# Performance work log

Hardware: AMD Instinct MI355X
Metric: run time of the kernel (lower is better)

Reference implementation:

```python
import jax, jax.numpy as jnp
import numpy as np

B, D, A, R = 256, 1024, 1024, 8  # batch, feat_dim, ada_dim, rank
I = A  # inter_dim defaults to ada_dim
LN_EPS = 1e-5


def setup_inputs() -> dict:
    key = jax.random.key(0)
    ks = jax.random.split(key, 5)
    return {
        "x": jax.random.normal(ks[0], (B, D), jnp.float32),
        "ada_emb": jax.random.normal(ks[1], (B, A), jnp.float32),
        "base_layer": jax.random.normal(ks[2], (D, D), jnp.float32) * 0.02,
        "ln_gamma": jnp.ones((A,), jnp.float32),
        "ln_beta": jnp.zeros((A,), jnp.float32),
        "W1": jax.random.normal(ks[3], (A, I), jnp.float32) * 0.02,
        "b1": jnp.zeros((I,), jnp.float32),
        "W2": jax.random.normal(ks[4], (I, D * R * 2), jnp.float32) * 0.02,
        "b2": jnp.zeros((D * R * 2,), jnp.float32),
    }


def reference(x, ada_emb, base_layer, ln_gamma, ln_beta, W1, b1, W2, b2):
    Bc, Dc = x.shape
    # norm_cond: LayerNorm over ada_dim
    mu = jnp.mean(ada_emb, axis=-1, keepdims=True)
    var = jnp.var(ada_emb, axis=-1, keepdims=True)
    cond = (ada_emb - mu) * jax.lax.rsqrt(var + LN_EPS) * ln_gamma + ln_beta
    # gen_weight: Linear -> GELU (exact, erf) -> Linear
    h = jax.nn.gelu(cond @ W1 + b1, approximate=False)
    w = h @ W2 + b2                      # [B, 2*D*R]
    x_a, x_b = jnp.split(w, 2, axis=-1)
    x_a = x_a.reshape(Bc, Dc, R)         # [B, D, R]
    x_b = x_b.reshape(Bc, Dc, R)         # [B, D, R]
    # per-sample low-rank weight added to the shared base layer
    layer = base_layer[None, :, :] + jnp.einsum('bdr,bkr->bdk', x_a, x_b)  # [B, D, D]
    out = jnp.einsum('bc,bco->bo', x, layer)
    return x + out  # residual=True
```

## Files before the change

kernel.cpp:

```cpp
#include <hip/hip_runtime.h>
#include <math.h>

#define BB 256
#define DD 1024
#define AA 1024
#define RR 8
#define II 1024
#define NOUT (2*DD*RR)
#define LN_EPS 1e-5f

typedef __attribute__((ext_vector_type(8))) short bf16x8;
typedef __attribute__((ext_vector_type(8))) unsigned short ushort8;
typedef __attribute__((ext_vector_type(4))) float f32x4;

typedef const __attribute__((address_space(1))) unsigned int gu32_t;
typedef __attribute__((address_space(3))) unsigned int lu32_t;

__device__ __forceinline__ void glds16(void* lds, const void* g) {
    __builtin_amdgcn_global_load_lds((gu32_t*)g, (lu32_t*)lds, 16, 0, 0);
}

__device__ __forceinline__ f32x4 mfma16(bf16x8 a, bf16x8 b, f32x4 c) {
    return __builtin_amdgcn_mfma_f32_16x16x32_bf16(a, b, c, 0, 0, 0);
}

__device__ __forceinline__ unsigned short f2bf(float x) {
    unsigned int u = __float_as_uint(x);
    unsigned int r = (u + 0x7fffu + ((u >> 16) & 1u)) >> 16;
    return (unsigned short)r;
}
__device__ __forceinline__ float bf2f(unsigned short b) {
    return __uint_as_float(((unsigned int)b) << 16);
}
__device__ __forceinline__ void split2(float x, unsigned short& hi, unsigned short& lo) {
    hi = f2bf(x);
    lo = f2bf(x - bf2f(hi));
}

__device__ __forceinline__ float gelu_exact(float v) {
    return 0.5f * v * (1.0f + erff(v * 0.70710678118654752f));
}

__device__ __forceinline__ void bar() {
    __builtin_amdgcn_sched_barrier(0);
    __builtin_amdgcn_s_barrier();
    __builtin_amdgcn_sched_barrier(0);
}

__global__ __launch_bounds__(256) void ln_split_kernel(const float* __restrict__ ada,
                                                       const float* __restrict__ xp,
                                                       const float* __restrict__ gamma,
                                                       const float* __restrict__ beta,
                                                       char* __restrict__ c_t,
                                                       char* __restrict__ x_t) {
    const int b = blockIdx.x;
    const int tid = threadIdx.x;
    const float4 v = ((const float4*)(ada + (size_t)b * AA))[tid];

    float s  = v.x + v.y + v.z + v.w;
    float ss = v.x * v.x + v.y * v.y + v.z * v.z + v.w * v.w;
    #pragma unroll
    for (int off = 32; off; off >>= 1) {
        s  += __shfl_down(s, off);
        ss += __shfl_down(ss, off);
    }
    __shared__ float red[2][4];
    const int wid = tid >> 6, lane = tid & 63;
    if (lane == 0) { red[0][wid] = s; red[1][wid] = ss; }
    __syncthreads();
    __shared__ float stats[2];
    if (tid == 0) {
        float S  = red[0][0] + red[0][1] + red[0][2] + red[0][3];
        float SS = red[1][0] + red[1][1] + red[1][2] + red[1][3];
        float mu  = S * (1.0f / AA);
        float var = SS * (1.0f / AA) - mu * mu;
        stats[0] = mu;
        stats[1] = rsqrtf(var + LN_EPS);
    }
    __syncthreads();
    const float mu = stats[0], inv = stats[1];
    const float4 g  = ((const float4*)gamma)[tid];
    const float4 be = ((const float4*)beta)[tid];

    const int k0 = tid * 4;
    const int mbh = (b >> 4) & 1;
    const size_t img = ((size_t)(b >> 5) * 16 + (k0 >> 6)) * 8192;
    const int inoff = ((k0 >> 3) & 7) * 256 + (b & 15) * 16 + (k0 & 7) * 2;

    float o[4];
    o[0] = (v.x - mu) * inv * g.x + be.x;
    o[1] = (v.y - mu) * inv * g.y + be.y;
    o[2] = (v.z - mu) * inv * g.z + be.z;
    o[3] = (v.w - mu) * inv * g.w + be.w;
    ushort4 H, L;
    split2(o[0], H.x, L.x); split2(o[1], H.y, L.y);
    split2(o[2], H.z, L.z); split2(o[3], H.w, L.w);
    *(ushort4*)(c_t + img + (0 * 2 + mbh) * 2048 + inoff) = H;
    *(ushort4*)(c_t + img + (1 * 2 + mbh) * 2048 + inoff) = L;

    const float4 xv = ((const float4*)(xp + (size_t)b * DD))[tid];
    split2(xv.x, H.x, L.x); split2(xv.y, H.y, L.y);
    split2(xv.z, H.z, L.z); split2(xv.w, H.w, L.w);
    *(ushort4*)(x_t + img + (0 * 2 + mbh) * 2048 + inoff) = H;
    *(ushort4*)(x_t + img + (1 * 2 + mbh) * 2048 + inoff) = L;
}

__global__ __launch_bounds__(256) void gemm_small(const char* __restrict__ x_t,
                                                  const char* __restrict__ c_t,
                                                  const float* __restrict__ base,
                                                  const float* __restrict__ W1,
                                                  const float* __restrict__ b1,
                                                  float* __restrict__ outy,
                                                  char* __restrict__ h_t) {
    __shared__ __align__(16) char As[2][8192];
    __shared__ __align__(16) char Bs[2][16384];

    const int z = blockIdx.z;
    const char* __restrict__ At = z ? c_t : x_t;
    const float* __restrict__ Bsrc = z ? W1 : base;

    const int tid = threadIdx.x;
    const int bn = blockIdx.x * 64;
    const int bm = blockIdx.y * 32;
    const int wid = tid >> 6, l = tid & 63;
    const int kg = l >> 4, lr16 = (l & 15) * 16;

    f32x4 acc[2];
    acc[0] = (f32x4)0.0f; acc[1] = (f32x4)0.0f;

    const int sn = tid & 63;
    const int sk0 = (tid >> 6) * 16;
    const int s_nb = sn >> 4, s_l16 = (sn & 15) * 16;

    float v[16];

    #define SB_LOAD(KT)                                                          \
        _Pragma("unroll")                                                        \
        for (int j = 0; j < 16; j++)                                             \
            v[j] = Bsrc[(size_t)((KT) * 64 + sk0 + j) * 1024 + bn + sn];

    #define SB_WRITE(BUF)                                                        \
        _Pragma("unroll")                                                        \
        for (int h2 = 0; h2 < 2; h2++) {                                         \
            const int kidx = (sk0 >> 3) + h2;                                    \
            ushort8 H, L;                                                        \
            _Pragma("unroll")                                                    \
            for (int j = 0; j < 8; j++) { unsigned short hh, ll;                 \
                split2(v[h2 * 8 + j], hh, ll); H[j] = hh; L[j] = ll; }           \
            *(ushort8*)(Bs[BUF] + ((0*4 + s_nb)*8 + kidx)*256 + s_l16) = H;      \
            *(ushort8*)(Bs[BUF] + ((1*4 + s_nb)*8 + kidx)*256 + s_l16) = L;      \
        }

    #define SA_GLDS(BUF, KT)                                                     \
        {                                                                        \
            const char* ib = At + ((size_t)(bm >> 5) * 16 + (KT)) * 8192;        \
            _Pragma("unroll")                                                    \
            for (int c = 0; c < 2; c++) {                                        \
                const int ch = wid * 2 + c;                                      \
                glds16(As[BUF] + ch * 1024, ib + ch * 1024 + l * 16);            \
            }                                                                    \
        }

    #define S_COMPUTE(BUF)                                                       \
        _Pragma("unroll")                                                        \
        for (int s2 = 0; s2 < 2; s2++) {                                         \
            bf16x8 a[2][2], bbf[2];                                              \
            _Pragma("unroll")                                                    \
            for (int pl = 0; pl < 2; pl++) {                                     \
                _Pragma("unroll")                                                \
                for (int mi = 0; mi < 2; mi++)                                   \
                    a[pl][mi] = *(const bf16x8*)(As[BUF] +                       \
                        ((pl*2 + mi)*8 + s2*4 + kg)*256 + lr16);                 \
                bbf[pl] = *(const bf16x8*)(Bs[BUF] +                             \
                        ((pl*4 + wid)*8 + s2*4 + kg)*256 + lr16);                \
            }                                                                    \
            __builtin_amdgcn_s_setprio(1);                                       \
            _Pragma("unroll")                                                    \
            for (int mi = 0; mi < 2; mi++) {                                     \
                acc[mi] = mfma16(a[0][mi], bbf[0], acc[mi]);                     \
                acc[mi] = mfma16(a[0][mi], bbf[1], acc[mi]);                     \
                acc[mi] = mfma16(a[1][mi], bbf[0], acc[mi]);                     \
            }                                                                    \
            __builtin_amdgcn_s_setprio(0);                                       \
        }

    SB_LOAD(0);
    SA_GLDS(0, 0);
    SB_WRITE(0);
    asm volatile("s_waitcnt lgkmcnt(0)" ::: "memory");
    bar();

    for (int t = 0; t < 16; ++t) {
        const int cur = t & 1;
        if (t < 15) {
            SB_LOAD(t + 1);
            SA_GLDS(cur ^ 1, t + 1);
            asm volatile("s_waitcnt vmcnt(18)" ::: "memory");
        } else {
            asm volatile("s_waitcnt vmcnt(0)" ::: "memory");
        }
        bar();
        S_COMPUTE(cur);
        if (t < 15) {
            SB_WRITE(cur ^ 1);
        }
        asm volatile("s_waitcnt lgkmcnt(0)" ::: "memory");
        bar();
    }

    #pragma unroll
    for (int mi = 0; mi < 2; mi++) {
        const int row0 = bm + mi * 16 + kg * 4;
        const int col  = bn + wid * 16 + (l & 15);
        #pragma unroll
        for (int j = 0; j < 4; j++) {
            float val = acc[mi][j];
            const int row = row0 + j;
            if (z == 0) {
                outy[(size_t)row * 1024 + col] = val;
            } else {
                float g = gelu_exact(val + b1[col]);
                unsigned short hi, lo;
                split2(g, hi, lo);
                char* ib = h_t + ((size_t)(row >> 7) * 32 + (col >> 5)) * 16384;
                const int inoff = (((row >> 4) & 7) * 4 + ((col >> 3) & 3)) * 256
                                + (row & 15) * 16 + (col & 7) * 2;
                *(unsigned short*)(ib + 0 * 8192 + inoff) = hi;
                *(unsigned short*)(ib + 1 * 8192 + inoff) = lo;
            }
        }
    }
    #undef SB_LOAD
    #undef SB_WRITE
    #undef SA_GLDS
    #undef S_COMPUTE
}

__global__ __launch_bounds__(256) void gemm_big(const char* __restrict__ h_t,
                                                const float* __restrict__ Bm,
                                                const float* __restrict__ bias,
                                                float* __restrict__ Cm) {
    __shared__ __align__(16) char As[2][16384];
    __shared__ __align__(16) char Bs[2][8192];

    const int hw = blockIdx.x;
    const int swz = ((hw & 7) << 6) + (hw >> 3);
    const int bn = (swz >> 1) * 64;
    const int bm = (swz & 1) * 128;

    const int tid = threadIdx.x;
    const int wid = tid >> 6, l = tid & 63;
    const int wm = wid >> 1, wn = wid & 1;
    const int kg = l >> 4, lr16 = (l & 15) * 16;

    f32x4 acc[4][2];
    #pragma unroll
    for (int i = 0; i < 4; i++) { acc[i][0] = (f32x4)0.0f; acc[i][1] = (f32x4)0.0f; }

    const int sn = tid & 63;
    const int skc = tid >> 6;
    const int s_nb = sn >> 4, s_l16 = (sn & 15) * 16;

    float v[8];

    #define GB_LOAD(KT)                                                          \
        _Pragma("unroll")                                                        \
        for (int j = 0; j < 8; j++)                                              \
            v[j] = Bm[(size_t)((KT) * 32 + skc * 8 + j) * NOUT + bn + sn];

    #define GB_WRITE(BUF)                                                        \
        {                                                                        \
            ushort8 H, L;                                                        \
            _Pragma("unroll")                                                    \
            for (int j = 0; j < 8; j++) { unsigned short hh, ll;                 \
                split2(v[j], hh, ll); H[j] = hh; L[j] = ll; }                    \
            *(ushort8*)(Bs[BUF] + ((0*4 + s_nb)*4 + skc)*256 + s_l16) = H;       \
            *(ushort8*)(Bs[BUF] + ((1*4 + s_nb)*4 + skc)*256 + s_l16) = L;       \
        }

    #define GA_GLDS(BUF, KT)                                                     \
        {                                                                        \
            const char* ib = h_t + ((size_t)(bm >> 7) * 32 + (KT)) * 16384;      \
            _Pragma("unroll")                                                    \
            for (int c = 0; c < 4; c++) {                                        \
                const int ch = wid * 4 + c;                                      \
                glds16(As[BUF] + ch * 1024, ib + ch * 1024 + l * 16);            \
            }                                                                    \
        }

    #define G_COMPUTE(BUF)                                                       \
        {                                                                        \
            bf16x8 a[2][4], bbf[2][2];                                           \
            _Pragma("unroll")                                                    \
            for (int pl = 0; pl < 2; pl++) {                                     \
                _Pragma("unroll")                                                \
                for (int mi = 0; mi < 4; mi++)                                   \
                    a[pl][mi] = *(const bf16x8*)(As[BUF] +                       \
                        ((pl*8 + wm*4 + mi)*4 + kg)*256 + lr16);                 \
                _Pragma("unroll")                                                \
                for (int ni = 0; ni < 2; ni++)                                   \
                    bbf[pl][ni] = *(const bf16x8*)(Bs[BUF] +                     \
                        ((pl*4 + wn*2 + ni)*4 + kg)*256 + lr16);                 \
            }                                                                    \
            __builtin_amdgcn_s_setprio(1);                                       \
            _Pragma("unroll")                                                    \
            for (int mi = 0; mi < 4; mi++) {                                     \
                _Pragma("unroll")                                                \
                for (int ni = 0; ni < 2; ni++) {                                 \
                    acc[mi][ni] = mfma16(a[0][mi], bbf[0][ni], acc[mi][ni]);     \
                    acc[mi][ni] = mfma16(a[0][mi], bbf[1][ni], acc[mi][ni]);     \
                    acc[mi][ni] = mfma16(a[1][mi], bbf[0][ni], acc[mi][ni]);     \
                }                                                                \
            }                                                                    \
            __builtin_amdgcn_s_setprio(0);                                       \
        }

    GB_LOAD(0);
    GA_GLDS(0, 0);
    GB_WRITE(0);
    asm volatile("s_waitcnt lgkmcnt(0)" ::: "memory");
    bar();

    for (int t = 0; t < 32; ++t) {
        const int cur = t & 1;
        if (t < 31) {
            GB_LOAD(t + 1);
            GA_GLDS(cur ^ 1, t + 1);
            asm volatile("s_waitcnt vmcnt(12)" ::: "memory");
        } else {
            asm volatile("s_waitcnt vmcnt(0)" ::: "memory");
        }
        bar();
        G_COMPUTE(cur);
        if (t < 31) {
            GB_WRITE(cur ^ 1);
        }
        asm volatile("s_waitcnt lgkmcnt(0)" ::: "memory");
        bar();
    }

    #pragma unroll
    for (int mi = 0; mi < 4; mi++) {
        #pragma unroll
        for (int ni = 0; ni < 2; ni++) {
            const int row0 = bm + wm * 64 + mi * 16 + kg * 4;
            const int col  = bn + wn * 32 + ni * 16 + (l & 15);
            const float bv = bias[col];
            #pragma unroll
            for (int j = 0; j < 4; j++)
                Cm[(size_t)(row0 + j) * NOUT + col] = acc[mi][ni][j] + bv;
        }
    }
    #undef GB_LOAD
    #undef GB_WRITE
    #undef GA_GLDS
    #undef G_COMPUTE
}

__global__ __launch_bounds__(256) void tail_kernel(const float* __restrict__ x,
                                                   const float* __restrict__ w,
                                                   float* __restrict__ out) {
    const int b = blockIdx.x;
    const int tid = threadIdx.x;
    const float* wa = w + (size_t)b * NOUT;
    const float4 xv = ((const float4*)(x + (size_t)b * DD))[tid];
    const float xs[4] = {xv.x, xv.y, xv.z, xv.w};

    float acc[RR] = {};
    #pragma unroll
    for (int i = 0; i < 4; i++) {
        const int c = tid * 4 + i;
        const float4 w0 = *(const float4*)&wa[c * RR];
        const float4 w1 = *(const float4*)&wa[c * RR + 4];
        acc[0] = fmaf(xs[i], w0.x, acc[0]);
        acc[1] = fmaf(xs[i], w0.y, acc[1]);
        acc[2] = fmaf(xs[i], w0.z, acc[2]);
        acc[3] = fmaf(xs[i], w0.w, acc[3]);
        acc[4] = fmaf(xs[i], w1.x, acc[4]);
        acc[5] = fmaf(xs[i], w1.y, acc[5]);
        acc[6] = fmaf(xs[i], w1.z, acc[6]);
        acc[7] = fmaf(xs[i], w1.w, acc[7]);
    }
    __shared__ float red[4][RR];
    __shared__ float trs[RR];
    const int wid = tid >> 6, lane = tid & 63;
    #pragma unroll
    for (int r = 0; r < RR; r++) {
        float vv = acc[r];
        #pragma unroll
        for (int off = 32; off; off >>= 1) vv += __shfl_down(vv, off);
        if (lane == 0) red[wid][r] = vv;
    }
    __syncthreads();
    if (tid < RR) trs[tid] = red[0][tid] + red[1][tid] + red[2][tid] + red[3][tid];
    __syncthreads();

    float tr[RR];
    #pragma unroll
    for (int r = 0; r < RR; r++) tr[r] = trs[r];

    const float* wb = wa + DD * RR;
    const int o0 = tid * 4;
    const float4 yv = *(const float4*)&out[(size_t)b * DD + o0];

    float vals[4];
    #pragma unroll
    for (int i = 0; i < 4; i++) {
        const float4 w0 = *(const float4*)&wb[(o0 + i) * RR];
        const float4 w1 = *(const float4*)&wb[(o0 + i) * RR + 4];
        vals[i] = tr[0] * w0.x + tr[1] * w0.y + tr[2] * w0.z + tr[3] * w0.w
                + tr[4] * w1.x + tr[5] * w1.y + tr[6] * w1.z + tr[7] * w1.w;
    }
    float4 o;
    o.x = xv.x + yv.x + vals[0];
    o.y = xv.y + yv.y + vals[1];
    o.z = xv.z + yv.z + vals[2];
    o.w = xv.w + yv.w + vals[3];
    *(float4*)&out[(size_t)b * DD + o0] = o;
}

extern "C" void kernel_launch(void* const* d_in, const int* in_sizes, int n_in,
                              void* d_out, int out_size, void* d_ws, size_t ws_size,
                              hipStream_t stream) {
    const float* x     = (const float*)d_in[0];
    const float* ada   = (const float*)d_in[1];
    const float* base  = (const float*)d_in[2];
    const float* gamma = (const float*)d_in[3];
    const float* beta  = (const float*)d_in[4];
    const float* W1    = (const float*)d_in[5];
    const float* b1    = (const float*)d_in[6];
    const float* W2    = (const float*)d_in[7];
    const float* b2    = (const float*)d_in[8];
    float* out = (float*)d_out;

    char* wsb = (char*)d_ws;
    float* w  = (float*)(wsb);
    char* h_t = wsb + 16777216;
    char* x_t = wsb + 17825792;
    char* c_t = wsb + 18874368;

    ln_split_kernel<<<BB, 256, 0, stream>>>(ada, x, gamma, beta, c_t, x_t);

    gemm_small<<<dim3(1024 / 64, BB / 32, 2), 256, 0, stream>>>(
        x_t, c_t, base, W1, b1, out, h_t);

    gemm_big<<<512, 256, 0, stream>>>(h_t, W2, b2, w);

    tail_kernel<<<BB, 256, 0, stream>>>(x, w, out);
}
```

Measured before the change: 178.6 us.

## Fuse four kernels into one cooperative persistent kernel with grid syncs

Replaces the four separate launches (layernorm/split, small GEMMs, big GEMM, tail) with a single cooperative kernel of 512 blocks that runs each stage in turn, separated by grid-wide syncs. Shared memory is unioned into one 48KB buffer, and launch bounds ask for 2 blocks per CU. The aim is to remove per-launch overhead and inter-kernel gaps. In exchange it adds grid barrier cost and idles half the blocks in the stages that use only 256, and occupancy limits could lower GEMM throughput.

```diff
diff --git a/kernel.cpp b/kernel.cpp
--- a/kernel.cpp
+++ b/kernel.cpp
@@ -1,5 +1,8 @@
 #include <hip/hip_runtime.h>
+#include <hip/hip_cooperative_groups.h>
 #include <math.h>
+
+namespace cg = cooperative_groups;
 
 #define BB 256
 #define DD 1024
@@ -16,8 +19,8 @@
 typedef const __attribute__((address_space(1))) unsigned int gu32_t;
 typedef __attribute__((address_space(3))) unsigned int lu32_t;
 
-__device__ __forceinline__ void glds16(void* lds, const void* g) {
-    __builtin_amdgcn_global_load_lds((gu32_t*)g, (lu32_t*)lds, 16, 0, 0);
+__device__ __forceinline__ void glds16(void* ldsp, const void* g) {
+    __builtin_amdgcn_global_load_lds((gu32_t*)g, (lu32_t*)ldsp, 16, 0, 0);
 }
 
 __device__ __forceinline__ f32x4 mfma16(bf16x8 a, bf16x8 b, f32x4 c) {
@@ -47,376 +50,366 @@
     __builtin_amdgcn_sched_barrier(0);
 }
 
-__global__ __launch_bounds__(256) void ln_split_kernel(const float* __restrict__ ada,
-                                                       const float* __restrict__ xp,
-                                                       const float* __restrict__ gamma,
-                                                       const float* __restrict__ beta,
-                                                       char* __restrict__ c_t,
-                                                       char* __restrict__ x_t) {
-    const int b = blockIdx.x;
+__global__ __launch_bounds__(256, 2) void fused_all(
+    const float* __restrict__ xp, const float* __restrict__ ada,
+    const float* __restrict__ base, const float* __restrict__ gamma,
+    const float* __restrict__ beta, const float* __restrict__ W1,
+    const float* __restrict__ b1, const float* __restrict__ W2,
+    const float* __restrict__ b2, float* __restrict__ out,
+    float* __restrict__ w, char* __restrict__ h_t,
+    char* __restrict__ x_t, char* __restrict__ c_t)
+{
+    __shared__ __align__(16) char lds[49152];
+    cg::grid_group grid = cg::this_grid();
+    const int bid = blockIdx.x;
     const int tid = threadIdx.x;
-    const float4 v = ((const float4*)(ada + (size_t)b * AA))[tid];
-
-    float s  = v.x + v.y + v.z + v.w;
-    float ss = v.x * v.x + v.y * v.y + v.z * v.z + v.w * v.w;
-    #pragma unroll
-    for (int off = 32; off; off >>= 1) {
-        s  += __shfl_down(s, off);
-        ss += __shfl_down(ss, off);
+
+    if (bid < 256) {
+        const int b = bid;
+        float* red   = (float*)lds;
+        float* stats = (float*)lds + 8;
+        const float4 v = ((const float4*)(ada + (size_t)b * AA))[tid];
+
+        float s  = v.x + v.y + v.z + v.w;
+        float ss = v.x * v.x + v.y * v.y + v.z * v.z + v.w * v.w;
+        #pragma unroll
+        for (int off = 32; off; off >>= 1) {
+            s  += __shfl_down(s, off);
+            ss += __shfl_down(ss, off);
+        }
+        const int wd = tid >> 6, lane = tid & 63;
+        if (lane == 0) { red[wd] = s; red[4 + wd] = ss; }
+        __syncthreads();
+        if (tid == 0) {
+            float S  = red[0] + red[1] + red[2] + red[3];
+            float SS = red[4] + red[5] + red[6] + red[7];
+            float mu  = S * (1.0f / AA);
+            float var = SS * (1.0f / AA) - mu * mu;
+            stats[0] = mu;
+            stats[1] = rsqrtf(var + LN_EPS);
+        }
+        __syncthreads();
+        const float mu = stats[0], inv = stats[1];
+        const float4 g  = ((const float4*)gamma)[tid];
+        const float4 be = ((const float4*)beta)[tid];
+
+        const int k0 = tid * 4;
+        const int mbh = (b >> 4) & 1;
+        const size_t img = ((size_t)(b >> 5) * 16 + (k0 >> 6)) * 8192;
+        const int inoff = ((k0 >> 3) & 7) * 256 + (b & 15) * 16 + (k0 & 7) * 2;
+
+        float o[4];
+        o[0] = (v.x - mu) * inv * g.x + be.x;
+        o[1] = (v.y - mu) * inv * g.y + be.y;
+        o[2] = (v.z - mu) * inv * g.z + be.z;
+        o[3] = (v.w - mu) * inv * g.w + be.w;
+        ushort4 H, L;
+        split2(o[0], H.x, L.x); split2(o[1], H.y, L.y);
+        split2(o[2], H.z, L.z); split2(o[3], H.w, L.w);
+        *(ushort4*)(c_t + img + (0 * 2 + mbh) * 2048 + inoff) = H;
+        *(ushort4*)(c_t + img + (1 * 2 + mbh) * 2048 + inoff) = L;
+
+        const float4 xv = ((const float4*)(xp + (size_t)b * DD))[tid];
+        split2(xv.x, H.x, L.x); split2(xv.y, H.y, L.y);
+        split2(xv.z, H.z, L.z); split2(xv.w, H.w, L.w);
+        *(ushort4*)(x_t + img + (0 * 2 + mbh) * 2048 + inoff) = H;
+        *(ushort4*)(x_t + img + (1 * 2 + mbh) * 2048 + inoff) = L;
     }
-    __shared__ float red[2][4];
-    const int wid = tid >> 6, lane = tid & 63;
-    if (lane == 0) { red[0][wid] = s; red[1][wid] = ss; }
-    __syncthreads();
-    __shared__ float stats[2];
-    if (tid == 0) {
-        float S  = red[0][0] + red[0][1] + red[0][2] + red[0][3];
-        float SS = red[1][0] + red[1][1] + red[1][2] + red[1][3];
-        float mu  = S * (1.0f / AA);
-        float var = SS * (1.0f / AA) - mu * mu;
-        stats[0] = mu;
-        stats[1] = rsqrtf(var + LN_EPS);
-    }
-    __syncthreads();
-    const float mu = stats[0], inv = stats[1];
-    const float4 g  = ((const float4*)gamma)[tid];
-    const float4 be = ((const float4*)beta)[tid];
-
-    const int k0 = tid * 4;
-    const int mbh = (b >> 4) & 1;
-    const size_t img = ((size_t)(b >> 5) * 16 + (k0 >> 6)) * 8192;
-    const int inoff = ((k0 >> 3) & 7) * 256 + (b & 15) * 16 + (k0 & 7) * 2;
-
-    float o[4];
-    o[0] = (v.x - mu) * inv * g.x + be.x;
-    o[1] = (v.y - mu) * inv * g.y + be.y;
-    o[2] = (v.z - mu) * inv * g.z + be.z;
-    o[3] = (v.w - mu) * inv * g.w + be.w;
-    ushort4 H, L;
-    split2(o[0], H.x, L.x); split2(o[1], H.y, L.y);
-    split2(o[2], H.z, L.z); split2(o[3], H.w, L.w);
-    *(ushort4*)(c_t + img + (0 * 2 + mbh) * 2048 + inoff) = H;
-    *(ushort4*)(c_t + img + (1 * 2 + mbh) * 2048 + inoff) = L;
-
-    const float4 xv = ((const float4*)(xp + (size_t)b * DD))[tid];
-    split2(xv.x, H.x, L.x); split2(xv.y, H.y, L.y);
-    split2(xv.z, H.z, L.z); split2(xv.w, H.w, L.w);
-    *(ushort4*)(x_t + img + (0 * 2 + mbh) * 2048 + inoff) = H;
-    *(ushort4*)(x_t + img + (1 * 2 + mbh) * 2048 + inoff) = L;
-}
-
-__global__ __launch_bounds__(256) void gemm_small(const char* __restrict__ x_t,
-                                                  const char* __restrict__ c_t,
-                                                  const float* __restrict__ base,
-                                                  const float* __restrict__ W1,
-                                                  const float* __restrict__ b1,
-                                                  float* __restrict__ outy,
-                                                  char* __restrict__ h_t) {
-    __shared__ __align__(16) char As[2][8192];
-    __shared__ __align__(16) char Bs[2][16384];
-
-    const int z = blockIdx.z;
-    const char* __restrict__ At = z ? c_t : x_t;
-    const float* __restrict__ Bsrc = z ? W1 : base;
-
-    const int tid = threadIdx.x;
-    const int bn = blockIdx.x * 64;
-    const int bm = blockIdx.y * 32;
-    const int wid = tid >> 6, l = tid & 63;
-    const int kg = l >> 4, lr16 = (l & 15) * 16;
-
-    f32x4 acc[2];
-    acc[0] = (f32x4)0.0f; acc[1] = (f32x4)0.0f;
-
-    const int sn = tid & 63;
-    const int sk0 = (tid >> 6) * 16;
-    const int s_nb = sn >> 4, s_l16 = (sn & 15) * 16;
-
-    float v[16];
-
-    #define SB_LOAD(KT)                                                          \
-        _Pragma("unroll")                                                        \
-        for (int j = 0; j < 16; j++)                                             \
-            v[j] = Bsrc[(size_t)((KT) * 64 + sk0 + j) * 1024 + bn + sn];
-
-    #define SB_WRITE(BUF)                                                        \
-        _Pragma("unroll")                                                        \
-        for (int h2 = 0; h2 < 2; h2++) {                                         \
-            const int kidx = (sk0 >> 3) + h2;                                    \
-            ushort8 H, L;                                                        \
-            _Pragma("unroll")                                                    \
-            for (int j = 0; j < 8; j++) { unsigned short hh, ll;                 \
-                split2(v[h2 * 8 + j], hh, ll); H[j] = hh; L[j] = ll; }           \
-            *(ushort8*)(Bs[BUF] + ((0*4 + s_nb)*8 + kidx)*256 + s_l16) = H;      \
-            *(ushort8*)(Bs[BUF] + ((1*4 + s_nb)*8 + kidx)*256 + s_l16) = L;      \
-        }
-
-    #define SA_GLDS(BUF, KT)                                                     \
-        {                                                                        \
-            const char* ib = At + ((size_t)(bm >> 5) * 16 + (KT)) * 8192;        \
-            _Pragma("unroll")                                                    \
-            for (int c = 0; c < 2; c++) {                                        \
-                const int ch = wid * 2 + c;                                      \
-                glds16(As[BUF] + ch * 1024, ib + ch * 1024 + l * 16);            \
-            }                                                                    \
-        }
-
-    #define S_COMPUTE(BUF)                                                       \
-        _Pragma("unroll")                                                        \
-        for (int s2 = 0; s2 < 2; s2++) {                                         \
-            bf16x8 a[2][2], bbf[2];                                              \
-            _Pragma("unroll")                                                    \
-            for (int pl = 0; pl < 2; pl++) {                                     \
-                _Pragma("unroll")                                                \
-                for (int mi = 0; mi < 2; mi++)                                   \
-                    a[pl][mi] = *(const bf16x8*)(As[BUF] +                       \
-                        ((pl*2 + mi)*8 + s2*4 + kg)*256 + lr16);                 \
-                bbf[pl] = *(const bf16x8*)(Bs[BUF] +                             \
-                        ((pl*4 + wid)*8 + s2*4 + kg)*256 + lr16);                \
-            }                                                                    \
-            __builtin_amdgcn_s_setprio(1);                                       \
-            _Pragma("unroll")                                                    \
-            for (int mi = 0; mi < 2; mi++) {                                     \
-                acc[mi] = mfma16(a[0][mi], bbf[0], acc[mi]);                     \
-                acc[mi] = mfma16(a[0][mi], bbf[1], acc[mi]);                     \
-                acc[mi] = mfma16(a[1][mi], bbf[0], acc[mi]);                     \
-            }                                                                    \
-            __builtin_amdgcn_s_setprio(0);                                       \
-        }
-
-    SB_LOAD(0);
-    SA_GLDS(0, 0);
-    SB_WRITE(0);
-    asm volatile("s_waitcnt lgkmcnt(0)" ::: "memory");
-    bar();
-
-    for (int t = 0; t < 16; ++t) {
-        const int cur = t & 1;
-        if (t < 15) {
-            SB_LOAD(t + 1);
-            SA_GLDS(cur ^ 1, t + 1);
-            asm volatile("s_waitcnt vmcnt(18)" ::: "memory");
-        } else {
-            asm volatile("s_waitcnt vmcnt(0)" ::: "memory");
-        }
-        bar();
-        S_COMPUTE(cur);
-        if (t < 15) {
-            SB_WRITE(cur ^ 1);
-        }
+    grid.sync();
+
+    if (bid < 256) {
+        const int z = bid >> 7;
+        const char* __restrict__ At = z ? c_t : x_t;
+        const float* __restrict__ Bsrc = z ? W1 : base;
+        const int bn = (bid & 15) * 64;
+        const int bm = ((bid >> 4) & 7) * 32;
+        const int wd = tid >> 6, l = tid & 63;
+        const int kg = l >> 4, lr16 = (l & 15) * 16;
+
+        f32x4 acc[2];
+        acc[0] = (f32x4)0.0f; acc[1] = (f32x4)0.0f;
+
+        const int sn = tid & 63;
+        const int sk0 = (tid >> 6) * 16;
+        const int s_nb = sn >> 4, s_l16 = (sn & 15) * 16;
+        float v[16];
+
+        #define SB_LOAD(KT)                                                          \
+            _Pragma("unroll")                                                        \
+            for (int j = 0; j < 16; j++)                                             \
+                v[j] = Bsrc[(size_t)((KT) * 64 + sk0 + j) * 1024 + bn + sn];
+
+        #define SB_WRITE(BUF)                                                        \
+            _Pragma("unroll")                                                        \
+            for (int h2 = 0; h2 < 2; h2++) {                                         \
+                const int kidx = (sk0 >> 3) + h2;                                    \
+                ushort8 H, L;                                                        \
+                _Pragma("unroll")                                                    \
+                for (int j = 0; j < 8; j++) { unsigned short hh, ll;                 \
+                    split2(v[h2 * 8 + j], hh, ll); H[j] = hh; L[j] = ll; }           \
+                *(ushort8*)(lds + 16384 + (BUF)*16384 + ((0*4 + s_nb)*8 + kidx)*256 + s_l16) = H; \
+                *(ushort8*)(lds + 16384 + (BUF)*16384 + ((1*4 + s_nb)*8 + kidx)*256 + s_l16) = L; \
+            }
+
+        #define SA_GLDS(BUF, KT)                                                     \
+            {                                                                        \
+                const char* ib = At + ((size_t)(bm >> 5) * 16 + (KT)) * 8192;        \
+                _Pragma("unroll")                                                    \
+                for (int c = 0; c < 2; c++) {                                        \
+                    const int ch = wd * 2 + c;                                       \
+                    glds16(lds + (BUF)*8192 + ch * 1024, ib + ch * 1024 + l * 16);   \
+                }                                                                    \
+            }
+
+        #define S_COMPUTE(BUF)                                                       \
+            _Pragma("unroll")                                                        \
+            for (int s2 = 0; s2 < 2; s2++) {                                         \
+                bf16x8 a[2][2], bbf[2];                                              \
+                _Pragma("unroll")                                                    \
+                for (int pl = 0; pl < 2; pl++) {                                     \
+                    _Pragma("unroll")                                                \
+                    for (int mi = 0; mi < 2; mi++)                                   \
+                        a[pl][mi] = *(const bf16x8*)(lds + (BUF)*8192 +              \
+                            ((pl*2 + mi)*8 + s2*4 + kg)*256 + lr16);                 \
+                    bbf[pl] = *(const bf16x8*)(lds + 16384 + (BUF)*16384 +           \
+                            ((pl*4 + wd)*8 + s2*4 + kg)*256 + lr16);                 \
+                }                                                                    \
+                __builtin_amdgcn_s_setprio(1);                                       \
+                _Pragma("unroll")                                                    \
+                for (int mi = 0; mi < 2; mi++) {                                     \
+                    acc[mi] = mfma16(a[0][mi], bbf[0], acc[mi]);                     \
+                    acc[mi] = mfma16(a[0][mi], bbf[1], acc[mi]);                     \
+                    acc[mi] = mfma16(a[1][mi], bbf[0], acc[mi]);                     \
+                }                                                                    \
+                __builtin_amdgcn_s_setprio(0);                                       \
+            }
+
+        SB_LOAD(0);
+        SA_GLDS(0, 0);
+        SB_WRITE(0);
         asm volatile("s_waitcnt lgkmcnt(0)" ::: "memory");
         bar();
+
+        for (int t = 0; t < 16; ++t) {
+            const int cur = t & 1;
+            if (t < 15) {
+                SB_LOAD(t + 1);
+                SA_GLDS(cur ^ 1, t + 1);
+                asm volatile("s_waitcnt vmcnt(18)" ::: "memory");
+            } else {
+                asm volatile("s_waitcnt vmcnt(0)" ::: "memory");
+            }
+            bar();
+            S_COMPUTE(cur);
+            if (t < 15) {
+                SB_WRITE(cur ^ 1);
+            }
+            asm volatile("s_waitcnt lgkmcnt(0)" ::: "memory");
+            bar();
+        }
+
+        #pragma unroll
+        for (int mi = 0; mi < 2; mi++) {
+            const int row0 = bm + mi * 16 + kg * 4;
+            const int col  = bn + wd * 16 + (l & 15);
+            #pragma unroll
+            for (int j = 0; j < 4; j++) {
+                float val = acc[mi][j];
+                const int row = row0 + j;
+                if (z == 0) {
+                    out[(size_t)row * 1024 + col] = val;
+                } else {
+                    float gv = gelu_exact(val + b1[col]);
+                    unsigned short hi, lo;
+                    split2(gv, hi, lo);
+                    char* ib = h_t + ((size_t)(row >> 7) * 32 + (col >> 5)) * 16384;
+                    const int inoff = (((row >> 4) & 7) * 4 + ((col >> 3) & 3)) * 256
+                                    + (row & 15) * 16 + (col & 7) * 2;
+                    *(unsigned short*)(ib + 0 * 8192 + inoff) = hi;
+                    *(unsigned short*)(ib + 1 * 8192 + inoff) = lo;
+                }
+            }
+        }
+        #undef SB_LOAD
+        #undef SB_WRITE
+        #undef SA_GLDS
+        #undef S_COMPUTE
     }
-
-    #pragma unroll
-    for (int mi = 0; mi < 2; mi++) {
-        const int row0 = bm + mi * 16 + kg * 4;
-        const int col  = bn + wid * 16 + (l & 15);
-        #pragma unroll
-        for (int j = 0; j < 4; j++) {
-            float val = acc[mi][j];
-            const int row = row0 + j;
-            if (z == 0) {
-                outy[(size_t)row * 1024 + col] = val;
-            } else {
-                float g = gelu_exact(val + b1[col]);
-                unsigned short hi, lo;
-                split2(g, hi, lo);
-                char* ib = h_t + ((size_t)(row >> 7) * 32 + (col >> 5)) * 16384;
-                const int inoff = (((row >> 4) & 7) * 4 + ((col >> 3) & 3)) * 256
-                                + (row & 15) * 16 + (col & 7) * 2;
-                *(unsigned short*)(ib + 0 * 8192 + inoff) = hi;
-                *(unsigned short*)(ib + 1 * 8192 + inoff) = lo;
-            }
-        }
-    }
-    #undef SB_LOAD
-    #undef SB_WRITE
-    #undef SA_GLDS
-    #undef S_COMPUTE
-}
-
-__global__ __launch_bounds__(256) void gemm_big(const char* __restrict__ h_t,
-                                                const float* __restrict__ Bm,
-                                                const float* __restrict__ bias,
-                                                float* __restrict__ Cm) {
-    __shared__ __align__(16) char As[2][16384];
-    __shared__ __align__(16) char Bs[2][8192];
-
-    const int hw = blockIdx.x;
-    const int swz = ((hw & 7) << 6) + (hw >> 3);
-    const int bn = (swz >> 1) * 64;
-    const int bm = (swz & 1) * 128;
-
-    const int tid = threadIdx.x;
-    const int wid = tid >> 6, l = tid & 63;
-    const int wm = wid >> 1, wn = wid & 1;
-    const int kg = l >> 4, lr16 = (l & 15) * 16;
-
-    f32x4 acc[4][2];
-    #pragma unroll
-    for (int i = 0; i < 4; i++) { acc[i][0] = (f32x4)0.0f; acc[i][1] = (f32x4)0.0f; }
-
-    const int sn = tid & 63;
-    const int skc = tid >> 6;
-    const int s_nb = sn >> 4, s_l16 = (sn & 15) * 16;
-
-    float v[8];
-
-    #define GB_LOAD(KT)                                                          \
-        _Pragma("unroll")                                                        \
-        for (int j = 0; j < 8; j++)                                              \
-            v[j] = Bm[(size_t)((KT) * 32 + skc * 8 + j) * NOUT + bn + sn];
-
-    #define GB_WRITE(BUF)                                                        \
-        {                                                                        \
-            ushort8 H, L;                                                        \
-            _Pragma("unroll")                                                    \
-            for (int j = 0; j < 8; j++) { unsigned short hh, ll;                 \
-                split2(v[j], hh, ll); H[j] = hh; L[j] = ll; }                    \
-            *(ushort8*)(Bs[BUF] + ((0*4 + s_nb)*4 + skc)*256 + s_l16) = H;       \
-            *(ushort8*)(Bs[BUF] + ((1*4 + s_nb)*4 + skc)*256 + s_l16) = L;       \
-        }
-
-    #define GA_GLDS(BUF, KT)                                                     \
-        {                                                                        \
-            const char* ib = h_t + ((size_t)(bm >> 7) * 32 + (KT)) * 16384;      \
-            _Pragma("unroll")                                                    \
-            for (int c = 0; c < 4; c++) {                                        \
-                const int ch = wid * 4 + c;                                      \
-                glds16(As[BUF] + ch * 1024, ib + ch * 1024 + l * 16);            \
-            }                                                                    \
-        }
-
-    #define G_COMPUTE(BUF)                                                       \
-        {                                                                        \
-            bf16x8 a[2][4], bbf[2][2];                                           \
-            _Pragma("unroll")                                                    \
-            for (int pl = 0; pl < 2; pl++) {                                     \
-                _Pragma("unroll")                                                \
-                for (int mi = 0; mi < 4; mi++)                                   \
-                    a[pl][mi] = *(const bf16x8*)(As[BUF] +                       \
-                        ((pl*8 + wm*4 + mi)*4 + kg)*256 + lr16);                 \
-                _Pragma("unroll")                                                \
-                for (int ni = 0; ni < 2; ni++)                                   \
-                    bbf[pl][ni] = *(const bf16x8*)(Bs[BUF] +                     \
-                        ((pl*4 + wn*2 + ni)*4 + kg)*256 + lr16);                 \
-            }                                                                    \
-            __builtin_amdgcn_s_setprio(1);                                       \
-            _Pragma("unroll")                                                    \
-            for (int mi = 0; mi < 4; mi++) {                                     \
-                _Pragma("unroll")                                                \
-                for (int ni = 0; ni < 2; ni++) {                                 \
-                    acc[mi][ni] = mfma16(a[0][mi], bbf[0][ni], acc[mi][ni]);     \
-                    acc[mi][ni] = mfma16(a[0][mi], bbf[1][ni], acc[mi][ni]);     \
-                    acc[mi][ni] = mfma16(a[1][mi], bbf[0][ni], acc[mi][ni]);     \
-                }                                                                \
-            }                                                                    \
-            __builtin_amdgcn_s_setprio(0);                                       \
-        }
-
-    GB_LOAD(0);
-    GA_GLDS(0, 0);
-    GB_WRITE(0);
-    asm volatile("s_waitcnt lgkmcnt(0)" ::: "memory");
-    bar();
-
-    for (int t = 0; t < 32; ++t) {
-        const int cur = t & 1;
-        if (t < 31) {
-            GB_LOAD(t + 1);
-            GA_GLDS(cur ^ 1, t + 1);
-            asm volatile("s_waitcnt vmcnt(12)" ::: "memory");
-        } else {
-            asm volatile("s_waitcnt vmcnt(0)" ::: "memory");
-        }
-        bar();
-        G_COMPUTE(cur);
-        if (t < 31) {
-            GB_WRITE(cur ^ 1);
-        }
+    grid.sync();
+
+    {
+        const int hw = bid;
+        const int swz = ((hw & 7) << 6) + (hw >> 3);
+        const int bn = (swz >> 1) * 64;
+        const int bm = (swz & 1) * 128;
+
+        const int wd = tid >> 6, l = tid & 63;
+        const int wm = wd >> 1, wn = wd & 1;
+        const int kg = l >> 4, lr16 = (l & 15) * 16;
+
+        f32x4 acc[4][2];
+        #pragma unroll
+        for (int i = 0; i < 4; i++) { acc[i][0] = (f32x4)0.0f; acc[i][1] = (f32x4)0.0f; }
+
+        const int sn = tid & 63;
+        const int skc = tid >> 6;
+        const int s_nb = sn >> 4, s_l16 = (sn & 15) * 16;
+        float v[8];
+
+        #define GB_LOAD(KT)                                                          \
+            _Pragma("unroll")                                                        \
+            for (int j = 0; j < 8; j++)                                              \
+                v[j] = W2[(size_t)((KT) * 32 + skc * 8 + j) * NOUT + bn + sn];
+
+        #define GB_WRITE(BUF)                                                        \
+            {                                                                        \
+                ushort8 H, L;                                                        \
+                _Pragma("unroll")                                                    \
+                for (int j = 0; j < 8; j++) { unsigned short hh, ll;                 \
+                    split2(v[j], hh, ll); H[j] = hh; L[j] = ll; }                    \
+                *(ushort8*)(lds + 32768 + (BUF)*8192 + ((0*4 + s_nb)*4 + skc)*256 + s_l16) = H; \
+                *(ushort8*)(lds + 32768 + (BUF)*8192 + ((1*4 + s_nb)*4 + skc)*256 + s_l16) = L; \
+            }
+
+        #define GA_GLDS(BUF, KT)                                                     \
+            {                                                                        \
+                const char* ib = h_t + ((size_t)(bm >> 7) * 32 + (KT)) * 16384;      \
+                _Pragma("unroll")                                                    \
+                for (int c = 0; c < 4; c++) {                                        \
+                    const int ch = wd * 4 + c;                                       \
+                    glds16(lds + (BUF)*16384 + ch * 1024, ib + ch * 1024 + l * 16);  \
+                }                                                                    \
+            }
+
+        #define G_COMPUTE(BUF)                                                       \
+            {                                                                        \
+                bf16x8 a[2][4], bbf[2][2];                                           \
+                _Pragma("unroll")                                                    \
+                for (int pl = 0; pl < 2; pl++) {                                     \
+                    _Pragma("unroll")                                                \
+                    for (int mi = 0; mi < 4; mi++)                                   \
+                        a[pl][mi] = *(const bf16x8*)(lds + (BUF)*16384 +             \
+                            ((pl*8 + wm*4 + mi)*4 + kg)*256 + lr16);                 \
+                    _Pragma("unroll")                                                \
+                    for (int ni = 0; ni < 2; ni++)                                   \
+                        bbf[pl][ni] = *(const bf16x8*)(lds + 32768 + (BUF)*8192 +    \
+                            ((pl*4 + wn*2 + ni)*4 + kg)*256 + lr16);                 \
+                }                                                                    \
+                __builtin_amdgcn_s_setprio(1);                                       \
+                _Pragma("unroll")                                                    \
+                for (int mi = 0; mi < 4; mi++) {                                     \
+                    _Pragma("unroll")                                                \
+                    for (int ni = 0; ni < 2; ni++) {                                 \
+                        acc[mi][ni] = mfma16(a[0][mi], bbf[0][ni], acc[mi][ni]);     \
+                        acc[mi][ni] = mfma16(a[0][mi], bbf[1][ni], acc[mi][ni]);     \
+                        acc[mi][ni] = mfma16(a[1][mi], bbf[0][ni], acc[mi][ni]);     \
+                    }                                                                \
+                }                                                                    \
+                __builtin_amdgcn_s_setprio(0);                                       \
+            }
+
+        GB_LOAD(0);
+        GA_GLDS(0, 0);
+        GB_WRITE(0);
         asm volatile("s_waitcnt lgkmcnt(0)" ::: "memory");
         bar();
+
+        for (int t = 0; t < 32; ++t) {
+            const int cur = t & 1;
+            if (t < 31) {
+                GB_LOAD(t + 1);
+                GA_GLDS(cur ^ 1, t + 1);
+                asm volatile("s_waitcnt vmcnt(12)" ::: "memory");
+            } else {
+                asm volatile("s_waitcnt vmcnt(0)" ::: "memory");
+            }
+            bar();
+            G_COMPUTE(cur);
+            if (t < 31) {
+                GB_WRITE(cur ^ 1);
+            }
+            asm volatile("s_waitcnt lgkmcnt(0)" ::: "memory");
+            bar();
+        }
+
+        #pragma unroll
+        for (int mi = 0; mi < 4; mi++) {
+            #pragma unroll
+            for (int ni = 0; ni < 2; ni++) {
+                const int row0 = bm + wm * 64 + mi * 16 + kg * 4;
+                const int col  = bn + wn * 32 + ni * 16 + (l & 15);
+                const float bv = b2[col];
+                #pragma unroll
+                for (int j = 0; j < 4; j++)
+                    w[(size_t)(row0 + j) * NOUT + col] = acc[mi][ni][j] + bv;
+            }
+        }
+        #undef GB_LOAD
+        #undef GB_WRITE
+        #undef GA_GLDS
+        #undef G_COMPUTE
     }
-
-    #pragma unroll
-    for (int mi = 0; mi < 4; mi++) {
-        #pragma unroll
-        for (int ni = 0; ni < 2; ni++) {
-            const int row0 = bm + wm * 64 + mi * 16 + kg * 4;
-            const int col  = bn + wn * 32 + ni * 16 + (l & 15);
-            const float bv = bias[col];
+    grid.sync();
+
+    if (bid < 256) {
+        const int b = bid;
+        float* red = (float*)lds;
+        float* trs = (float*)lds + 32;
+        const float* wa = w + (size_t)b * NOUT;
+        const float4 xv = ((const float4*)(xp + (size_t)b * DD))[tid];
+        const float xs[4] = {xv.x, xv.y, xv.z, xv.w};
+
+        float acc[RR] = {};
+        #pragma unroll
+        for (int i = 0; i < 4; i++) {
+            const int c = tid * 4 + i;
+            const float4 w0 = *(const float4*)&wa[c * RR];
+            const float4 w1 = *(const float4*)&wa[c * RR + 4];
+            acc[0] = fmaf(xs[i], w0.x, acc[0]);
+            acc[1] = fmaf(xs[i], w0.y, acc[1]);
+            acc[2] = fmaf(xs[i], w0.z, acc[2]);
+            acc[3] = fmaf(xs[i], w0.w, acc[3]);
+            acc[4] = fmaf(xs[i], w1.x, acc[4]);
+            acc[5] = fmaf(xs[i], w1.y, acc[5]);
+            acc[6] = fmaf(xs[i], w1.z, acc[6]);
+            acc[7] = fmaf(xs[i], w1.w, acc[7]);
+        }
+        const int wd = tid >> 6, lane = tid & 63;
+        #pragma unroll
+        for (int r = 0; r < RR; r++) {
+            float vv = acc[r];
             #pragma unroll
-            for (int j = 0; j < 4; j++)
-                Cm[(size_t)(row0 + j) * NOUT + col] = acc[mi][ni][j] + bv;
-        }
+            for (int off = 32; off; off >>= 1) vv += __shfl_down(vv, off);
+            if (lane == 0) red[wd * RR + r] = vv;
+        }
+        __syncthreads();
+        if (tid < RR) trs[tid] = red[0 * RR + tid] + red[1 * RR + tid]
+                               + red[2 * RR + tid] + red[3 * RR + tid];
+        __syncthreads();
+
+        float tr[RR];
+        #pragma unroll
+        for (int r = 0; r < RR; r++) tr[r] = trs[r];
+
+        const float* wb = wa + DD * RR;
+        const int o0 = tid * 4;
+        const float4 yv = *(const float4*)&out[(size_t)b * DD + o0];
+
+        float vals[4];
+        #pragma unroll
+        for (int i = 0; i < 4; i++) {
+            const float4 w0 = *(const float4*)&wb[(o0 + i) * RR];
+            const float4 w1 = *(const float4*)&wb[(o0 + i) * RR + 4];
+            vals[i] = tr[0] * w0.x + tr[1] * w0.y + tr[2] * w0.z + tr[3] * w0.w
+                    + tr[4] * w1.x + tr[5] * w1.y + tr[6] * w1.z + tr[7] * w1.w;
+        }
+        float4 o;
+        o.x = xv.x + yv.x + vals[0];
+        o.y = xv.y + yv.y + vals[1];
+        o.z = xv.z + yv.z + vals[2];
+        o.w = xv.w + yv.w + vals[3];
+        *(float4*)&out[(size_t)b * DD + o0] = o;
     }
-    #undef GB_LOAD
-    #undef GB_WRITE
-    #undef GA_GLDS
-    #undef G_COMPUTE
-}
-
-__global__ __launch_bounds__(256) void tail_kernel(const float* __restrict__ x,
-                                                   const float* __restrict__ w,
-                                                   float* __restrict__ out) {
-    const int b = blockIdx.x;
-    const int tid = threadIdx.x;
-    const float* wa = w + (size_t)b * NOUT;
-    const float4 xv = ((const float4*)(x + (size_t)b * DD))[tid];
-    const float xs[4] = {xv.x, xv.y, xv.z, xv.w};
-
-    float acc[RR] = {};
-    #pragma unroll
-    for (int i = 0; i < 4; i++) {
-        const int c = tid * 4 + i;
-        const float4 w0 = *(const float4*)&wa[c * RR];
-        const float4 w1 = *(const float4*)&wa[c * RR + 4];
-        acc[0] = fmaf(xs[i], w0.x, acc[0]);
-        acc[1] = fmaf(xs[i], w0.y, acc[1]);
-        acc[2] = fmaf(xs[i], w0.z, acc[2]);
-        acc[3] = fmaf(xs[i], w0.w, acc[3]);
-        acc[4] = fmaf(xs[i], w1.x, acc[4]);
-        acc[5] = fmaf(xs[i], w1.y, acc[5]);
-        acc[6] = fmaf(xs[i], w1.z, acc[6]);
-        acc[7] = fmaf(xs[i], w1.w, acc[7]);
-    }
-    __shared__ float red[4][RR];
-    __shared__ float trs[RR];
-    const int wid = tid >> 6, lane = tid & 63;
-    #pragma unroll
-    for (int r = 0; r < RR; r++) {
-        float vv = acc[r];
-        #pragma unroll
-        for (int off = 32; off; off >>= 1) vv += __shfl_down(vv, off);
-        if (lane == 0) red[wid][r] = vv;
-    }
-    __syncthreads();
-    if (tid < RR) trs[tid] = red[0][tid] + red[1][tid] + red[2][tid] + red[3][tid];
-    __syncthreads();
-
-    float tr[RR];
-    #pragma unroll
-    for (int r = 0; r < RR; r++) tr[r] = trs[r];
-
-    const float* wb = wa + DD * RR;
-    const int o0 = tid * 4;
-    const float4 yv = *(const float4*)&out[(size_t)b * DD + o0];
-
-    float vals[4];
-    #pragma unroll
-    for (int i = 0; i < 4; i++) {
-        const float4 w0 = *(const float4*)&wb[(o0 + i) * RR];
-        const float4 w1 = *(const float4*)&wb[(o0 + i) * RR + 4];
-        vals[i] = tr[0] * w0.x + tr[1] * w0.y + tr[2] * w0.z + tr[3] * w0.w
-                + tr[4] * w1.x + tr[5] * w1.y + tr[6] * w1.z + tr[7] * w1.w;
-    }
-    float4 o;
-    o.x = xv.x + yv.x + vals[0];
-    o.y = xv.y + yv.y + vals[1];
-    o.z = xv.z + yv.z + vals[2];
-    o.w = xv.w + yv.w + vals[3];
-    *(float4*)&out[(size_t)b * DD + o0] = o;
 }
 
 extern "C" void kernel_launch(void* const* d_in, const int* in_sizes, int n_in,
@@ -439,12 +432,10 @@
     char* x_t = wsb + 17825792;
     char* c_t = wsb + 18874368;
 
-    ln_split_kernel<<<BB, 256, 0, stream>>>(ada, x, gamma, beta, c_t, x_t);
-
-    gemm_small<<<dim3(1024 / 64, BB / 32, 2), 256, 0, stream>>>(
-        x_t, c_t, base, W1, b1, out, h_t);
-
-    gemm_big<<<512, 256, 0, stream>>>(h_t, W2, b2, w);
-
-    tail_kernel<<<BB, 256, 0, stream>>>(x, w, out);
-}
+    void* args[] = { (void*)&x, (void*)&ada, (void*)&base, (void*)&gamma,
+                     (void*)&beta, (void*)&W1, (void*)&b1, (void*)&W2,
+                     (void*)&b2, (void*)&out, (void*)&w, (void*)&h_t,
+                     (void*)&x_t, (void*)&c_t };
+    hipLaunchCooperativeKernel((void*)fused_all, dim3(512), dim3(256),
+                               args, 0, stream);
+}
```

New measurement: 368.7 us. 2.06x slower.
